# Optimization experiments

Hardware: AMD Instinct MI355X
Metric: run time of the kernel (lower is better)

The kernel has to match this reference:

```python
import jax, jax.numpy as jnp
import numpy as np

NUM_HEADS = 16

def setup_inputs() -> dict:
    key = jax.random.key(0)
    k1, k2, k3, k4 = jax.random.split(key, 4)
    B, N, C = 4, 2048, 1024
    x = jax.random.normal(k1, (B, N, C), dtype=jnp.float32)
    xpos = jax.random.randint(k2, (B, N), 0, 2048, dtype=jnp.int64)
    Wqkv = jax.random.normal(k3, (C, 3 * C), dtype=jnp.float32) * (C ** -0.5)
    Wproj = jax.random.normal(k4, (C, C), dtype=jnp.float32) * (C ** -0.5)
    bproj = jnp.zeros((C,), dtype=jnp.float32)
    return {"x": x, "xpos": xpos, "Wqkv": Wqkv, "Wproj": Wproj, "bproj": bproj}

def reference(x, xpos, Wqkv, Wproj, bproj):
    # rope is None in this configuration, so xpos is unused (matches torch default path).
    B, N, C = x.shape
    H = NUM_HEADS
    Dh = C // H
    scale = Dh ** -0.5
    qkv = jnp.einsum('bnc,cd->bnd', x, Wqkv)              # [B, N, 3C]
    qkv = qkv.reshape(B, N, 3, H, Dh)
    q, k, v = qkv[:, :, 0], qkv[:, :, 1], qkv[:, :, 2]    # [B, N, H, Dh]
    scores = jnp.einsum('bnhd,bmhd->bhnm', q, k) * scale  # [B, H, N, N]
    attn = jax.nn.softmax(scores, axis=-1)
    out = jnp.einsum('bhnm,bmhd->bnhd', attn, v)          # [B, N, H, Dh]
    out = out.reshape(B, N, C)
    return jnp.einsum('bnc,cd->bnd', out, Wproj) + bproj
```

## Files before the change

kernel.cpp:

```cpp
#include <hip/hip_runtime.h>
#include <stdint.h>

#define DEVINL __device__ __forceinline__

typedef __bf16 bf16x8 __attribute__((ext_vector_type(8)));
typedef float f32x4 __attribute__((ext_vector_type(4)));
typedef float f32x16 __attribute__((ext_vector_type(16)));
typedef uint32_t u32x4 __attribute__((ext_vector_type(4)));

DEVINL uint16_t f2bf(float f) {
    uint32_t u = __builtin_bit_cast(uint32_t, f);
    uint32_t r = (u + 0x7FFFu + ((u >> 16) & 1u)) >> 16;
    return (uint16_t)r;
}

DEVINL bf16x8 ld8(const uint16_t* p) {
    u32x4 v = *(const u32x4*)p;
    return __builtin_bit_cast(bf16x8, v);
}

DEVINL void gload16(const void* g, void* l) {
    __builtin_amdgcn_global_load_lds(
        (const __attribute__((address_space(1))) uint32_t*)g,
        (__attribute__((address_space(3))) uint32_t*)l, 16, 0, 0);
}

DEVINL uint32_t cvtpk(float lo, float hi) {
    uint32_t r;
    asm("v_cvt_pk_bf16_f32 %0, %1, %2" : "=v"(r) : "v"(lo), "v"(hi));
    return r;
}

DEVINL float exp2_fast(float x) {
    float r;
    asm("v_exp_f32 %0, %1" : "=v"(r) : "v"(x));
    return r;
}

DEVINL void transW_body(const float* __restrict__ W, uint16_t* __restrict__ WT,
                        int Nn, int n0, int k0, int tid, uint16_t* t) {
#pragma unroll
    for (int i = 0; i < 4; ++i) {
        int c = tid + i * 256;
        int kr = c >> 4, nc = c & 15;
        float4 v = *(const float4*)(W + (size_t)(k0 + kr) * Nn + n0 + nc * 4);
        t[(nc * 4 + 0) * 65 + kr] = f2bf(v.x);
        t[(nc * 4 + 1) * 65 + kr] = f2bf(v.y);
        t[(nc * 4 + 2) * 65 + kr] = f2bf(v.z);
        t[(nc * 4 + 3) * 65 + kr] = f2bf(v.w);
    }
    __syncthreads();
#pragma unroll
    for (int i = 0; i < 2; ++i) {
        int c = tid + i * 256;
        int nr = c >> 3, kc = c & 7;
        union { uint16_t u[8]; u32x4 v; } o;
#pragma unroll
        for (int j = 0; j < 8; ++j) o.u[j] = t[nr * 65 + kc * 8 + j];
        *(u32x4*)(WT + (size_t)(n0 + nr) * 1024 + k0 + kc * 8) = o.v;
    }
}

__global__ void k_prep(const float* __restrict__ x, uint16_t* __restrict__ xb,
                       const float* __restrict__ Wqkv, uint16_t* __restrict__ wqkvT,
                       const float* __restrict__ Wproj, uint16_t* __restrict__ wprojT) {
    __shared__ uint16_t t[64 * 65];
    int bid = blockIdx.x;
    int tid = threadIdx.x;
    if (bid < 4096) {
        int i = bid * 256 + tid;
        const float4* src = (const float4*)x + (size_t)i * 2;
        float4 a = src[0], b = src[1];
        union { uint16_t u[8]; u32x4 v; } o;
        o.u[0] = f2bf(a.x); o.u[1] = f2bf(a.y); o.u[2] = f2bf(a.z); o.u[3] = f2bf(a.w);
        o.u[4] = f2bf(b.x); o.u[5] = f2bf(b.y); o.u[6] = f2bf(b.z); o.u[7] = f2bf(b.w);
        ((u32x4*)xb)[i] = o.v;
    } else if (bid < 4864) {
        int idx = bid - 4096;
        transW_body(Wqkv, wqkvT, 3072, (idx % 48) * 64, (idx / 48) * 64, tid, t);
    } else {
        int idx = bid - 4864;
        transW_body(Wproj, wprojT, 1024, (idx % 16) * 64, (idx / 16) * 64, tid, t);
    }
}

__global__ void k_transV(const uint16_t* __restrict__ vn, uint16_t* __restrict__ vt) {
    __shared__ uint16_t t[64 * 65];
    int bh = blockIdx.y;
    int n0 = blockIdx.x * 64;
    int tid = threadIdx.x;
#pragma unroll
    for (int i = 0; i < 2; ++i) {
        int c = tid + i * 256;
        int n = c >> 3, dc = c & 7;
        u32x4 vv = *(const u32x4*)(vn + ((size_t)bh * 2048 + n0 + n) * 64 + dc * 8);
        union { u32x4 v4; uint16_t u[8]; } in; in.v4 = vv;
#pragma unroll
        for (int j = 0; j < 8; ++j) t[(dc * 8 + j) * 65 + n] = in.u[j];
    }
    __syncthreads();
#pragma unroll
    for (int i = 0; i < 2; ++i) {
        int c = tid + i * 256;
        int dh = c >> 3, nc = c & 7;
        union { uint16_t u[8]; u32x4 v4; } o;
#pragma unroll
        for (int j = 0; j < 8; ++j) o.u[j] = t[dh * 65 + nc * 8 + j];
        *(u32x4*)(vt + ((size_t)bh * 64 + dh) * 2048 + n0 + nc * 8) = o.v4;
    }
}

template <int MODE>
__global__ __launch_bounds__(256) void k_gemm(
    const uint16_t* __restrict__ A, const uint16_t* __restrict__ BT,
    const float* __restrict__ bias,
    uint16_t* __restrict__ qo, uint16_t* __restrict__ ko, uint16_t* __restrict__ vo,
    float* __restrict__ out) {
    __shared__ uint16_t a_lds[128 * 64];
    __shared__ uint16_t b_lds[128 * 64];
    int tid = threadIdx.x;
    int w = tid >> 6, l = tid & 63;
    int l15 = l & 15, l4 = l >> 4;
    int m0 = blockIdx.y * 128, n0 = blockIdx.x * 128;
    int wr = w >> 1, wc = w & 1;
    f32x4 acc[4][4] = {};

    for (int kt = 0; kt < 16; ++kt) {
#pragma unroll
        for (int i = 0; i < 4; ++i) {
            int c = i * 256 + w * 64 + l;
            int row = c >> 3, slot = c & 7;
            int kc = slot ^ (row & 7);
            gload16(A + (size_t)(m0 + row) * 1024 + kt * 64 + kc * 8,
                    a_lds + (size_t)(i * 256 + w * 64) * 8);
            gload16(BT + (size_t)(n0 + row) * 1024 + kt * 64 + kc * 8,
                    b_lds + (size_t)(i * 256 + w * 64) * 8);
        }
        __syncthreads();
#pragma unroll
        for (int kkk = 0; kkk < 2; ++kkk) {
            bf16x8 af[4], bfr[4];
#pragma unroll
            for (int i = 0; i < 4; ++i) {
                int row = wr * 64 + i * 16 + l15;
                af[i] = ld8(a_lds + row * 64 + ((kkk * 4 + l4) ^ (row & 7)) * 8);
                int rowb = wc * 64 + i * 16 + l15;
                bfr[i] = ld8(b_lds + rowb * 64 + ((kkk * 4 + l4) ^ (rowb & 7)) * 8);
            }
#pragma unroll
            for (int i = 0; i < 4; ++i)
#pragma unroll
                for (int j = 0; j < 4; ++j)
                    acc[i][j] = __builtin_amdgcn_mfma_f32_16x16x32_bf16(
                        af[i], bfr[j], acc[i][j], 0, 0, 0);
        }
        __syncthreads();
    }

    if constexpr (MODE == 0) {
#pragma unroll
        for (int i = 0; i < 4; ++i)
#pragma unroll
            for (int j = 0; j < 4; ++j) {
                int d = n0 + wc * 64 + j * 16 + l15;
                int s = d >> 10, h = (d >> 6) & 15, dh = d & 63;
                uint16_t* dst0 = (s == 0) ? qo : (s == 1) ? ko : vo;
                float sc = (s == 0) ? 0.18033688011112042f : 1.0f;
#pragma unroll
                for (int r = 0; r < 4; ++r) {
                    int m = m0 + wr * 64 + i * 16 + l4 * 4 + r;
                    int b = m >> 11, n = m & 2047;
                    dst0[((size_t)(b * 16 + h) * 2048 + n) * 64 + dh] = f2bf(acc[i][j][r] * sc);
                }
            }
    } else {
#pragma unroll
        for (int j = 0; j < 4; ++j) {
            int d = n0 + wc * 64 + j * 16 + l15;
            float bv = bias[d];
#pragma unroll
            for (int i = 0; i < 4; ++i)
#pragma unroll
                for (int r = 0; r < 4; ++r) {
                    int m = m0 + wr * 64 + i * 16 + l4 * 4 + r;
                    out[(size_t)m * 1024 + d] = acc[i][j][r] + bv;
                }
        }
    }
}

__global__ __launch_bounds__(256) void k_attn(
    const uint16_t* __restrict__ q, const uint16_t* __restrict__ kk_,
    const uint16_t* __restrict__ vt, uint16_t* __restrict__ o) {
    __shared__ uint16_t k_lds[2][64 * 64];
    __shared__ uint16_t v_lds[2][64 * 64];
    int tid = threadIdx.x;
    int w = tid >> 6, l = tid & 63;
    int l31 = l & 31, g = l >> 5;
    int bid = blockIdx.x;
    int slot = bid >> 3;
    int bh = (bid & 7) * 8 + (slot >> 4);
    int qt = slot & 15;
    int qrow = qt * 128 + w * 32 + l31;
    const uint16_t* qb = q + ((size_t)bh * 2048 + qrow) * 64;
    const uint16_t* kbase = kk_ + (size_t)bh * 2048 * 64;
    const uint16_t* vbase = vt + (size_t)bh * 64 * 2048;

    bf16x8 qf[4];
#pragma unroll
    for (int kv = 0; kv < 4; ++kv) qf[kv] = ld8(qb + kv * 16 + g * 8);

    int c0 = w * 128 + l;
    int rr0 = c0 >> 3, sl0 = c0 & 7;
    int kc0 = sl0 ^ (rr0 & 7);
    int rr1 = rr0 + 8, kc1 = sl0 ^ (rr1 & 7);
    const uint16_t* kp0 = kbase + rr0 * 64 + kc0 * 8;
    const uint16_t* kp1 = kbase + rr1 * 64 + kc1 * 8;
    const uint16_t* vp0 = vbase + (size_t)rr0 * 2048 + kc0 * 8;
    const uint16_t* vp1 = vbase + (size_t)rr1 * 2048 + kc1 * 8;
    uint16_t* kd0 = k_lds[0] + w * 1024;
    uint16_t* kd1 = k_lds[1] + w * 1024;
    uint16_t* vd0 = v_lds[0] + w * 1024;
    uint16_t* vd1 = v_lds[1] + w * 1024;

    f32x16 oa[2] = {};
    float lsum = 0.f;

    auto stage = [&](uint16_t* kd, uint16_t* vd) {
        gload16(kp0, kd);       gload16(kp1, kd + 512);
        gload16(vp0, vd);       gload16(vp1, vd + 512);
        kp0 += 4096; kp1 += 4096; vp0 += 64; vp1 += 64;
    };

    stage(kd0, vd0);

    auto body = [&](int t, const uint16_t* kb, const uint16_t* vb,
                    uint16_t* kdn, uint16_t* vdn) {
        asm volatile("s_waitcnt vmcnt(2)\n\ts_barrier" ::: "memory");
        if (t < 31) stage(kdn, vdn);

        bf16x8 pfrag[4];
#pragma unroll
        for (int j = 0; j < 2; ++j) {
            int key = j * 32 + l31;
            f32x16 stj = {};
            __builtin_amdgcn_s_setprio(1);
#pragma unroll
            for (int kv = 0; kv < 4; ++kv) {
                bf16x8 kf = ld8(kb + key * 64 + ((2 * kv + g) ^ (key & 7)) * 8);
                stj = __builtin_amdgcn_mfma_f32_32x32x16_bf16(kf, qf[kv], stj, 0, 0, 0);
            }
            __builtin_amdgcn_s_setprio(0);
#pragma unroll
            for (int h = 0; h < 2; ++h) {
                float e[8];
#pragma unroll
                for (int jj = 0; jj < 8; ++jj) e[jj] = exp2_fast(stj[h * 8 + jj]);
                lsum += ((e[0] + e[1]) + (e[2] + e[3])) + ((e[4] + e[5]) + (e[6] + e[7]));
                uint32_t a0 = cvtpk(e[0], e[1]), a1 = cvtpk(e[2], e[3]);
                uint32_t b0 = cvtpk(e[4], e[5]), b1 = cvtpk(e[6], e[7]);
                auto r0 = __builtin_amdgcn_permlane32_swap(a0, b0, false, false);
                auto r1 = __builtin_amdgcn_permlane32_swap(a1, b1, false, false);
                u32x4 f;
                f[0] = r0[0]; f[1] = r1[0]; f[2] = r0[1]; f[3] = r1[1];
                pfrag[j * 2 + h] = __builtin_bit_cast(bf16x8, f);
            }
        }

        if (t < 31) asm volatile("s_waitcnt vmcnt(4)\n\ts_barrier" ::: "memory");
        else        asm volatile("s_waitcnt vmcnt(0)\n\ts_barrier" ::: "memory");

        __builtin_amdgcn_s_setprio(1);
#pragma unroll
        for (int kv = 0; kv < 4; ++kv) {
#pragma unroll
            for (int dt = 0; dt < 2; ++dt) {
                int dh = dt * 32 + l31;
                bf16x8 vf = ld8(vb + dh * 64 + ((2 * kv + g) ^ (dh & 7)) * 8);
                oa[dt] = __builtin_amdgcn_mfma_f32_32x32x16_bf16(vf, pfrag[kv], oa[dt], 0, 0, 0);
            }
        }
        __builtin_amdgcn_s_setprio(0);
    };

    for (int kt = 0; kt < 32; kt += 2) {
        body(kt,     k_lds[0], v_lds[0], kd1, vd1);
        body(kt + 1, k_lds[1], v_lds[1], kd0, vd0);
    }

    float ltot = lsum + __shfl_xor(lsum, 32, 64);
    float inv = 1.0f / ltot;
    int b = bh >> 4, h = bh & 15;
    uint16_t* ob = o + ((size_t)(b * 2048 + qrow)) * 1024 + h * 64;
#pragma unroll
    for (int dt = 0; dt < 2; ++dt)
#pragma unroll
        for (int rq = 0; rq < 4; ++rq) {
            union { uint16_t u[4]; uint2 v; } pk;
#pragma unroll
            for (int rr = 0; rr < 4; ++rr) pk.u[rr] = f2bf(oa[dt][rq * 4 + rr] * inv);
            int dh0 = dt * 32 + rq * 8 + g * 4;
            *(uint2*)(ob + dh0) = pk.v;
        }
}

extern "C" void kernel_launch(void* const* d_in, const int* in_sizes, int n_in,
                              void* d_out, int out_size, void* d_ws, size_t ws_size,
                              hipStream_t stream) {
    const float* x     = (const float*)d_in[0];
    const float* Wqkv  = (const float*)d_in[2];
    const float* Wproj = (const float*)d_in[3];
    const float* bproj = (const float*)d_in[4];
    float* out = (float*)d_out;

    char* ws = (char*)d_ws;
    uint16_t* xb     = (uint16_t*)(ws);
    uint16_t* wqkvT  = (uint16_t*)(ws + 16777216);
    uint16_t* wprojT = (uint16_t*)(ws + 23068672);
    uint16_t* qws    = (uint16_t*)(ws + 25165824);
    uint16_t* kws    = (uint16_t*)(ws + 41943040);
    uint16_t* vT     = (uint16_t*)(ws + 58720256);
    uint16_t* vnat   = (uint16_t*)(ws + 75497472);
    uint16_t* attnout = xb;

    k_prep<<<dim3(5120), dim3(256), 0, stream>>>(x, xb, Wqkv, wqkvT, Wproj, wprojT);
    k_gemm<0><<<dim3(24, 64), dim3(256), 0, stream>>>(xb, wqkvT, nullptr, qws, kws, vnat, nullptr);
    k_transV<<<dim3(32, 64), dim3(256), 0, stream>>>(vnat, vT);
    k_attn<<<dim3(1024), dim3(256), 0, stream>>>(qws, kws, vT, attnout);
    k_gemm<1><<<dim3(8, 64), dim3(256), 0, stream>>>(attnout, wprojT, bproj, nullptr, nullptr, nullptr, out);
}
```

Baseline: 211.1 us.

## Store K in MFMA fragment layout and load it straight into registers

The QKV GEMM epilogue now writes K in a blocked layout that matches the attention kernel's MFMA operand fragments. The attention kernel then loads each 64-key K tile directly from global memory into registers, dropping the K shared-memory buffers, their LDS reads and the barrier-guarded K staging. K loads for the next tile are issued after the current QK MFMAs, and the vmcnt waits are adjusted so only the V staging is waited on. In exchange, each of the four waves now fetches the whole K tile itself, which raises global/L2 traffic, and the loads depend on the compiler placing waits for register-destination loads well.

```diff
diff --git a/kernel.cpp b/kernel.cpp
--- a/kernel.cpp
+++ b/kernel.cpp
@@ -164,13 +164,20 @@
             for (int j = 0; j < 4; ++j) {
                 int d = n0 + wc * 64 + j * 16 + l15;
                 int s = d >> 10, h = (d >> 6) & 15, dh = d & 63;
-                uint16_t* dst0 = (s == 0) ? qo : (s == 1) ? ko : vo;
                 float sc = (s == 0) ? 0.18033688011112042f : 1.0f;
 #pragma unroll
                 for (int r = 0; r < 4; ++r) {
                     int m = m0 + wr * 64 + i * 16 + l4 * 4 + r;
                     int b = m >> 11, n = m & 2047;
-                    dst0[((size_t)(b * 16 + h) * 2048 + n) * 64 + dh] = f2bf(acc[i][j][r] * sc);
+                    int bh = b * 16 + h;
+                    uint16_t val = f2bf(acc[i][j][r] * sc);
+                    if (s == 1) {
+                        ko[(size_t)bh * 131072 + (size_t)(n >> 6) * 4096 +
+                           (dh >> 3) * 512 + (n & 63) * 8 + (dh & 7)] = val;
+                    } else {
+                        uint16_t* dst0 = (s == 0) ? qo : vo;
+                        dst0[((size_t)bh * 2048 + n) * 64 + dh] = val;
+                    }
                 }
             }
     } else {
@@ -190,9 +197,8 @@
 }
 
 __global__ __launch_bounds__(256) void k_attn(
-    const uint16_t* __restrict__ q, const uint16_t* __restrict__ kk_,
+    const uint16_t* __restrict__ q, const uint16_t* __restrict__ kf_,
     const uint16_t* __restrict__ vt, uint16_t* __restrict__ o) {
-    __shared__ uint16_t k_lds[2][64 * 64];
     __shared__ uint16_t v_lds[2][64 * 64];
     int tid = threadIdx.x;
     int w = tid >> 6, l = tid & 63;
@@ -203,8 +209,8 @@
     int qt = slot & 15;
     int qrow = qt * 128 + w * 32 + l31;
     const uint16_t* qb = q + ((size_t)bh * 2048 + qrow) * 64;
-    const uint16_t* kbase = kk_ + (size_t)bh * 2048 * 64;
     const uint16_t* vbase = vt + (size_t)bh * 64 * 2048;
+    const uint16_t* kfb = kf_ + (size_t)bh * 131072 + g * 512 + l31 * 8;
 
     bf16x8 qf[4];
 #pragma unroll
@@ -214,43 +220,46 @@
     int rr0 = c0 >> 3, sl0 = c0 & 7;
     int kc0 = sl0 ^ (rr0 & 7);
     int rr1 = rr0 + 8, kc1 = sl0 ^ (rr1 & 7);
-    const uint16_t* kp0 = kbase + rr0 * 64 + kc0 * 8;
-    const uint16_t* kp1 = kbase + rr1 * 64 + kc1 * 8;
     const uint16_t* vp0 = vbase + (size_t)rr0 * 2048 + kc0 * 8;
     const uint16_t* vp1 = vbase + (size_t)rr1 * 2048 + kc1 * 8;
-    uint16_t* kd0 = k_lds[0] + w * 1024;
-    uint16_t* kd1 = k_lds[1] + w * 1024;
     uint16_t* vd0 = v_lds[0] + w * 1024;
     uint16_t* vd1 = v_lds[1] + w * 1024;
 
+    bf16x8 kr[8];
+    auto loadK = [&](int t) {
+        const uint16_t* p = kfb + (size_t)t * 4096;
+        kr[0] = ld8(p);        kr[1] = ld8(p + 1024);
+        kr[2] = ld8(p + 2048); kr[3] = ld8(p + 3072);
+        kr[4] = ld8(p + 256);  kr[5] = ld8(p + 1280);
+        kr[6] = ld8(p + 2304); kr[7] = ld8(p + 3328);
+    };
+    auto stageV = [&](uint16_t* vd) {
+        gload16(vp0, vd); gload16(vp1, vd + 512);
+        vp0 += 64; vp1 += 64;
+    };
+
     f32x16 oa[2] = {};
     float lsum = 0.f;
 
-    auto stage = [&](uint16_t* kd, uint16_t* vd) {
-        gload16(kp0, kd);       gload16(kp1, kd + 512);
-        gload16(vp0, vd);       gload16(vp1, vd + 512);
-        kp0 += 4096; kp1 += 4096; vp0 += 64; vp1 += 64;
-    };
-
-    stage(kd0, vd0);
-
-    auto body = [&](int t, const uint16_t* kb, const uint16_t* vb,
-                    uint16_t* kdn, uint16_t* vdn) {
-        asm volatile("s_waitcnt vmcnt(2)\n\ts_barrier" ::: "memory");
-        if (t < 31) stage(kdn, vdn);
+    loadK(0);
+    stageV(vd0);
+
+    auto body = [&](int t, const uint16_t* vb, uint16_t* vdn) {
+        asm volatile("s_barrier" ::: "memory");
 
         bf16x8 pfrag[4];
 #pragma unroll
         for (int j = 0; j < 2; ++j) {
-            int key = j * 32 + l31;
             f32x16 stj = {};
             __builtin_amdgcn_s_setprio(1);
 #pragma unroll
-            for (int kv = 0; kv < 4; ++kv) {
-                bf16x8 kf = ld8(kb + key * 64 + ((2 * kv + g) ^ (key & 7)) * 8);
-                stj = __builtin_amdgcn_mfma_f32_32x32x16_bf16(kf, qf[kv], stj, 0, 0, 0);
-            }
+            for (int kv = 0; kv < 4; ++kv)
+                stj = __builtin_amdgcn_mfma_f32_32x32x16_bf16(kr[j * 4 + kv], qf[kv], stj, 0, 0, 0);
             __builtin_amdgcn_s_setprio(0);
+            if (j == 1 && t < 31) {
+                loadK(t + 1);
+                stageV(vdn);
+            }
 #pragma unroll
             for (int h = 0; h < 2; ++h) {
                 float e[8];
@@ -267,7 +276,7 @@
             }
         }
 
-        if (t < 31) asm volatile("s_waitcnt vmcnt(4)\n\ts_barrier" ::: "memory");
+        if (t < 31) asm volatile("s_waitcnt vmcnt(10)\n\ts_barrier" ::: "memory");
         else        asm volatile("s_waitcnt vmcnt(0)\n\ts_barrier" ::: "memory");
 
         __builtin_amdgcn_s_setprio(1);
@@ -284,8 +293,8 @@
     };
 
     for (int kt = 0; kt < 32; kt += 2) {
-        body(kt,     k_lds[0], v_lds[0], kd1, vd1);
-        body(kt + 1, k_lds[1], v_lds[1], kd0, vd0);
+        body(kt,     v_lds[0], vd1);
+        body(kt + 1, v_lds[1], vd0);
     }
 
     float ltot = lsum + __shfl_xor(lsum, 32, 64);
```

Measured after the change: 212.6 us. About the same (+0.7%).
